# Performance work log

Measured on AMD Instinct MI355X. Metric: run time of the kernel, lower is better.

The kernel has to match this reference:

```python
import jax, jax.numpy as jnp
import numpy as np

HEADS = 8
DIM_HEAD = 64
SCALE = DIM_HEAD ** (-0.5)


def setup_inputs() -> dict:
    key = jax.random.key(0)
    k1, k2, k3, k4 = jax.random.split(key, 4)
    B, H, W, n, dim = 2, 64, 64, 8, 512
    inner = HEADS * DIM_HEAD  # 512
    x = jax.random.normal(k1, (B, H, W, n, dim), dtype=jnp.float32)
    mask = jax.random.uniform(k2, (B, H, W, 1, n, n), dtype=jnp.float32)
    w_qkv = jax.random.normal(k3, (dim, 3 * inner), dtype=jnp.float32) * 0.02
    w_out = jax.random.normal(k4, (inner, dim), dtype=jnp.float32) * 0.02
    b_out = jnp.zeros((dim,), dtype=jnp.float32)
    return {"x": x, "mask": mask, "w_qkv": w_qkv, "w_out": w_out, "b_out": b_out}


def reference(x, mask, w_qkv, w_out, b_out):
    B, H, W, n, dim = x.shape
    inner = HEADS * DIM_HEAD
    qkv = x @ w_qkv  # [B,H,W,n,3*inner]
    q, k, v = jnp.split(qkv, 3, axis=-1)

    def to_heads(t):
        # 'B H W n (h d) -> B H W h n d'
        t = t.reshape(B, H, W, n, HEADS, DIM_HEAD)
        return jnp.swapaxes(t, 3, 4)

    q, k, v = to_heads(q), to_heads(k), to_heads(v)
    dots = jnp.einsum('bxyhnd,bxyhmd->bxyhnm', q, k) * SCALE
    dots = dots * mask  # multiplicative mask pre-softmax
    attn = jax.nn.softmax(dots, axis=-1)
    out = jnp.einsum('bxyhnm,bxyhmd->bxyhnd', attn, v)
    # 'B H W h n d -> B H W n (h d)'
    out = jnp.swapaxes(out, 3, 4).reshape(B, H, W, n, inner)
    return out @ w_out + b_out
```

## Files before the change

### kernel.cpp

```cpp
#include <hip/hip_runtime.h>
#include <hip/hip_bf16.h>

#define NROWS 65536
#define DIM   512
#define SCALE_ 0.125f

typedef short bf16x8 __attribute__((ext_vector_type(8)));
typedef unsigned short u16x8 __attribute__((ext_vector_type(8)));
typedef float f32x4 __attribute__((ext_vector_type(4)));

__device__ __forceinline__ unsigned short f2bf(float f) {
  union { float f; unsigned u; } v; v.f = f;
  unsigned r = v.u + 0x7FFFu + ((v.u >> 16) & 1u);
  return (unsigned short)(r >> 16);
}

#define GLL16(gptr, lptr) \
  __builtin_amdgcn_global_load_lds((const __attribute__((address_space(1))) void*)(gptr), \
                                   (__attribute__((address_space(3))) void*)(lptr), 16, 0, 0)

__global__ void prep_w_kernel(const float* __restrict__ wqkv,
                              const float* __restrict__ wout,
                              unsigned short* __restrict__ wqkvT,
                              unsigned short* __restrict__ woutT) {
  int idx = blockIdx.x * 256 + threadIdx.x;
  if (idx < 1536 * 512) {
    int j = idx >> 9, c = idx & 511;
    wqkvT[idx] = f2bf(wqkv[(size_t)c * 1536 + j]);
  } else {
    int k2 = idx - 1536 * 512;
    int n = k2 >> 9, c = k2 & 511;
    woutT[k2] = f2bf(wout[(size_t)c * 512 + n]);
  }
}

__global__ __launch_bounds__(256, 2)
void qkv_attn_kernel(const float* __restrict__ x,
                     const float* __restrict__ mask,
                     const unsigned short* __restrict__ wqkvT,
                     unsigned short* __restrict__ attn_out) {
  __shared__ __align__(16) unsigned char smem[81920];

  const int t = threadIdx.x;
  const int lane = t & 63, wave = t >> 6;
  const int wm = wave >> 1, wn = wave & 1;
  const int fr = lane & 15, fq = lane >> 4;
  const int l8 = lane >> 3;
  const int cswz = ((lane & 7) ^ l8) * 8;

  const int per = gridDim.x >> 3;
  const int lin = (blockIdx.x & 7) * per + (blockIdx.x >> 3);
  const int mtile = lin >> 3, head = lin & 7;
  const int r0 = mtile * 128;

  float mreg[2][4];
  #pragma unroll
  for (int pp = 0; pp < 2; ++pp) {
    int pair = wave * 2 + pp;
    #pragma unroll
    for (int r = 0; r < 4; ++r) {
      int row = fq * 4 + r;
      int Pg = mtile * 16 + pair * 2 + (row >> 3);
      mreg[pp][r] = mask[(size_t)Pg * 64 + (row & 7) * 8 + (fr & 7)];
    }
  }

  f32x4 acc[4][6];
  const f32x4 z4 = {0.f, 0.f, 0.f, 0.f};
  #pragma unroll
  for (int m = 0; m < 4; ++m)
    #pragma unroll
    for (int n = 0; n < 6; ++n) acc[m][n] = z4;

  float4 va[8];
  const int arow = t >> 4, aq = t & 15;
  const unsigned abyte = (unsigned)arow * 128 +
                         ((((unsigned)(aq >> 1)) << 4) ^ (((unsigned)(arow & 7)) << 4)) +
                         (unsigned)(aq & 1) * 8;

  auto LOAD_A = [&](int kt2) {
    const int k0 = kt2 * 64;
    const float* gx = x + (size_t)(r0 + arow) * 512 + k0 + aq * 4;
    #pragma unroll
    for (int i2 = 0; i2 < 8; ++i2)
      va[i2] = *(const float4*)(gx + (size_t)i2 * 16 * 512);
  };
  auto WRITE_A = [&](int buf) {
    unsigned char* base = smem + buf * 40960;
    #pragma unroll
    for (int i2 = 0; i2 < 8; ++i2) {
      ushort4 p;
      p.x = f2bf(va[i2].x); p.y = f2bf(va[i2].y);
      p.z = f2bf(va[i2].z); p.w = f2bf(va[i2].w);
      *(ushort4*)(base + abyte + (unsigned)i2 * 2048) = p;
    }
  };
  auto STAGE_B = [&](int buf, int kt2) {
    unsigned char* base = smem + buf * 40960 + 16384;
    const unsigned short* gB = wqkvT + kt2 * 64 + cswz;
    #pragma unroll
    for (int i = 0; i < 6; ++i) {
      int c = wave * 6 + i;
      int n = c * 8 + l8;
      int jg = ((n >> 6) << 9) + head * 64 + (n & 63);
      GLL16(gB + (size_t)jg * 512, base + c * 1024);
    }
  };

  LOAD_A(0);
  STAGE_B(0, 0);
  WRITE_A(0);
  asm volatile("s_waitcnt vmcnt(0)" ::: "memory");
  __syncthreads();
  int cur = 0;

  for (int kt = 0; kt < 8; ++kt) {
    if (kt < 7) { LOAD_A(kt + 1); STAGE_B(cur ^ 1, kt + 1); }
    unsigned char* Ab = smem + cur * 40960;
    unsigned char* Bb = Ab + 16384;
    const unsigned xr = ((unsigned)(fr & 7)) << 4;
    #pragma unroll
    for (int kk = 0; kk < 2; ++kk) {
      const unsigned ko = ((unsigned)(kk * 64 + fq * 16)) ^ xr;
      bf16x8 a[4], b[6];
      #pragma unroll
      for (int m = 0; m < 4; ++m)
        a[m] = *(const bf16x8*)(Ab + (unsigned)(wm * 64 + m * 16 + fr) * 128 + ko);
      #pragma unroll
      for (int n = 0; n < 6; ++n)
        b[n] = *(const bf16x8*)(Bb + (unsigned)(wn * 96 + n * 16 + fr) * 128 + ko);
      #pragma unroll
      for (int m = 0; m < 4; ++m)
        #pragma unroll
        for (int n = 0; n < 6; ++n)
          acc[m][n] = __builtin_amdgcn_mfma_f32_16x16x32_bf16(a[m], b[n], acc[m][n], 0, 0, 0);
    }
    if (kt < 7) WRITE_A(cur ^ 1);
    asm volatile("s_waitcnt vmcnt(0)" ::: "memory");
    __syncthreads();
    cur ^= 1;
  }

  unsigned short* Qs = (unsigned short*)smem;
  unsigned short* Ks = (unsigned short*)(smem + 16384);
  unsigned short* VT = (unsigned short*)(smem + 32768);
  unsigned short* Pl = (unsigned short*)(smem + 52224);

  {
    int d = t >> 2, q = t & 3;
    ushort4 z; z.x = 0; z.y = 0; z.z = 0; z.w = 0;
    *(ushort4*)(VT + d * 152 + 128 + q * 4) = z;
  }
  #pragma unroll
  for (int n = 0; n < 6; ++n) {
    int col = wn * 96 + n * 16 + fr;
    #pragma unroll
    for (int m = 0; m < 4; ++m) {
      if (col < 128) {
        unsigned short* T = (col < 64) ? Qs : Ks;
        unsigned cc = (unsigned)(col & 63);
        #pragma unroll
        for (int r = 0; r < 4; ++r) {
          int row = wm * 64 + m * 16 + fq * 4 + r;
          unsigned byte = (unsigned)row * 128 + ((cc * 2) ^ (((unsigned)(row & 7)) << 4));
          *(unsigned short*)((unsigned char*)T + byte) = f2bf(acc[m][n][r]);
        }
      } else {
        int d = col - 128;
        ushort4 p;
        p.x = f2bf(acc[m][n][0]); p.y = f2bf(acc[m][n][1]);
        p.z = f2bf(acc[m][n][2]); p.w = f2bf(acc[m][n][3]);
        *(ushort4*)(VT + d * 152 + (wm * 64 + m * 16 + fq * 4)) = p;
      }
    }
  }
  __syncthreads();

  #pragma unroll
  for (int pp = 0; pp < 2; ++pp) {
    const int pair = wave * 2 + pp;
    const unsigned rbyte = (unsigned)(pair * 16 + fr) * 128;
    const unsigned xrp = ((unsigned)(fr & 7)) << 4;
    f32x4 s = {0.f, 0.f, 0.f, 0.f};
    #pragma unroll
    for (int kk = 0; kk < 2; ++kk) {
      const unsigned ko = ((unsigned)(kk * 64 + fq * 16)) ^ xrp;
      bf16x8 qf = *(const bf16x8*)((unsigned char*)Qs + rbyte + ko);
      bf16x8 kf = *(const bf16x8*)((unsigned char*)Ks + rbyte + ko);
      s = __builtin_amdgcn_mfma_f32_16x16x32_bf16(qf, kf, s, 0, 0, 0);
    }
    float p4[4];
    #pragma unroll
    for (int r = 0; r < 4; ++r) {
      int row = fq * 4 + r;
      bool valid = (row >> 3) == (fr >> 3);
      p4[r] = valid ? s[r] * SCALE_ * mreg[pp][r] : -3.0e38f;
    }
    #pragma unroll
    for (int r = 0; r < 4; ++r) {
      float v = p4[r];
      float mx = v;
      mx = fmaxf(mx, __shfl_xor(mx, 1));
      mx = fmaxf(mx, __shfl_xor(mx, 2));
      mx = fmaxf(mx, __shfl_xor(mx, 4));
      float e = __expf(v - mx);
      float sm = e;
      sm += __shfl_xor(sm, 1);
      sm += __shfl_xor(sm, 2);
      sm += __shfl_xor(sm, 4);
      p4[r] = e / sm;
    }
    #pragma unroll
    for (int r = 0; r < 4; ++r) {
      int row = fq * 4 + r;
      bool valid = (row >> 3) == (fr >> 3);
      Pl[pair * 640 + row * 40 + fr] = valid ? f2bf(p4[r]) : (unsigned short)0;
      Pl[pair * 640 + row * 40 + 16 + fr] = 0;
    }
    #pragma unroll
    for (int dblk = 0; dblk < 4; ++dblk) {
      bf16x8 af = *(const bf16x8*)((unsigned char*)VT +
                    (unsigned)(dblk * 16 + fr) * 304 + (unsigned)(pair * 32 + fq * 16));
      bf16x8 bf = *(const bf16x8*)((unsigned char*)Pl +
                    (unsigned)pair * 1280 + (unsigned)fr * 80 + (unsigned)fq * 16);
      f32x4 o = {0.f, 0.f, 0.f, 0.f};
      o = __builtin_amdgcn_mfma_f32_16x16x32_bf16(af, bf, o, 0, 0, 0);
      ushort4 pk;
      pk.x = f2bf(o[0]); pk.y = f2bf(o[1]); pk.z = f2bf(o[2]); pk.w = f2bf(o[3]);
      *(ushort4*)(attn_out + (size_t)(r0 + pair * 16 + fr) * 512 +
                  head * 64 + dblk * 16 + fq * 4) = pk;
    }
  }
}

__global__ __launch_bounds__(256, 2)
void outproj_kernel(const unsigned short* __restrict__ attn,
                    const unsigned short* __restrict__ woutT,
                    const float* __restrict__ bias,
                    float* __restrict__ out) {
  __shared__ __align__(16) unsigned char smem[65536];
  const int t = threadIdx.x;
  const int lane = t & 63, wave = t >> 6;
  const int wm = wave >> 1, wn = wave & 1;
  const int fr = lane & 15, fq = lane >> 4;
  const int l8 = lane >> 3;
  const int cswz = ((lane & 7) ^ l8) * 8;

  const int per = gridDim.x >> 3;
  const int lin = (blockIdx.x & 7) * per + (blockIdx.x >> 3);
  const int mtile = lin >> 2, nt = lin & 3;
  const int r0 = mtile * 128, n0 = nt * 128;

  f32x4 acc[4][4];
  const f32x4 z4 = {0.f, 0.f, 0.f, 0.f};
  #pragma unroll
  for (int m = 0; m < 4; ++m)
    #pragma unroll
    for (int n = 0; n < 4; ++n) acc[m][n] = z4;

  auto STAGE = [&](int buf, int kt2) {
    unsigned char* base = smem + buf * 32768;
    const int k0 = kt2 * 64;
    const unsigned short* gA = attn  + (size_t)(r0 + l8) * 512 + k0 + cswz;
    const unsigned short* gB = woutT + (size_t)(n0 + l8) * 512 + k0 + cswz;
    #pragma unroll
    for (int i = 0; i < 4; ++i) {
      int c = wave * 4 + i;
      GLL16(gA + (size_t)c * 8 * 512, base + c * 1024);
      GLL16(gB + (size_t)c * 8 * 512, base + 16384 + c * 1024);
    }
  };

  STAGE(0, 0);
  asm volatile("s_waitcnt vmcnt(0)" ::: "memory");
  __syncthreads();
  int cur = 0;

  for (int kt = 0; kt < 8; ++kt) {
    if (kt < 7) STAGE(cur ^ 1, kt + 1);
    unsigned char* Ab = smem + cur * 32768;
    unsigned char* Bb = Ab + 16384;
    const unsigned xr = ((unsigned)(fr & 7)) << 4;
    #pragma unroll
    for (int kk = 0; kk < 2; ++kk) {
      const unsigned ko = ((unsigned)(kk * 64 + fq * 16)) ^ xr;
      bf16x8 a[4], b[4];
      #pragma unroll
      for (int m = 0; m < 4; ++m)
        a[m] = *(const bf16x8*)(Ab + (unsigned)(wm * 64 + m * 16 + fr) * 128 + ko);
      #pragma unroll
      for (int n = 0; n < 4; ++n)
        b[n] = *(const bf16x8*)(Bb + (unsigned)(wn * 64 + n * 16 + fr) * 128 + ko);
      #pragma unroll
      for (int m = 0; m < 4; ++m)
        #pragma unroll
        for (int n = 0; n < 4; ++n)
          acc[m][n] = __builtin_amdgcn_mfma_f32_16x16x32_bf16(a[m], b[n], acc[m][n], 0, 0, 0);
    }
    asm volatile("s_waitcnt vmcnt(0)" ::: "memory");
    __syncthreads();
    cur ^= 1;
  }
  #pragma unroll
  for (int n = 0; n < 4; ++n) {
    int col = n0 + wn * 64 + n * 16 + fr;
    float bv = bias[col];
    #pragma unroll
    for (int m = 0; m < 4; ++m) {
      #pragma unroll
      for (int j = 0; j < 4; ++j) {
        int row = r0 + wm * 64 + m * 16 + fq * 4 + j;
        out[(size_t)row * 512 + col] = acc[m][n][j] + bv;
      }
    }
  }
}

extern "C" void kernel_launch(void* const* d_in, const int* in_sizes, int n_in,
                              void* d_out, int out_size, void* d_ws, size_t ws_size,
                              hipStream_t stream) {
  const float* x    = (const float*)d_in[0];
  const float* mask = (const float*)d_in[1];
  const float* wqkv = (const float*)d_in[2];
  const float* wout = (const float*)d_in[3];
  const float* bias = (const float*)d_in[4];
  float* out = (float*)d_out;

  unsigned char* ws = (unsigned char*)d_ws;
  unsigned short* attn  = (unsigned short*)ws;
  unsigned short* wqkvT = (unsigned short*)(ws + 67108864);
  unsigned short* woutT = (unsigned short*)(ws + 67108864 + 1572864);

  prep_w_kernel<<<4096, 256, 0, stream>>>(wqkv, wout, wqkvT, woutT);
  qkv_attn_kernel<<<4096, 256, 0, stream>>>(x, mask, wqkvT, attn);
  outproj_kernel<<<2048, 256, 0, stream>>>(attn, woutT, bias, out);
}
```

Measured before the change: 278.5 us.

## Pre-convert x to bf16 and stream QKV tiles via 4-stage async LDS pipeline

```diff
diff --git a/kernel.cpp b/kernel.cpp
--- a/kernel.cpp
+++ b/kernel.cpp
@@ -19,23 +19,35 @@
   __builtin_amdgcn_global_load_lds((const __attribute__((address_space(1))) void*)(gptr), \
                                    (__attribute__((address_space(3))) void*)(lptr), 16, 0, 0)
 
-__global__ void prep_w_kernel(const float* __restrict__ wqkv,
-                              const float* __restrict__ wout,
-                              unsigned short* __restrict__ wqkvT,
-                              unsigned short* __restrict__ woutT) {
-  int idx = blockIdx.x * 256 + threadIdx.x;
-  if (idx < 1536 * 512) {
-    int j = idx >> 9, c = idx & 511;
-    wqkvT[idx] = f2bf(wqkv[(size_t)c * 1536 + j]);
+__global__ void prep_kernel(const float* __restrict__ x,
+                            const float* __restrict__ wqkv,
+                            const float* __restrict__ wout,
+                            unsigned short* __restrict__ xb,
+                            unsigned short* __restrict__ wqkvT,
+                            unsigned short* __restrict__ woutT) {
+  if (blockIdx.x < 16384) {
+    size_t i = ((size_t)blockIdx.x * 256 + threadIdx.x) * 8;
+    float4 a = *(const float4*)(x + i);
+    float4 b = *(const float4*)(x + i + 4);
+    u16x8 p;
+    p[0] = f2bf(a.x); p[1] = f2bf(a.y); p[2] = f2bf(a.z); p[3] = f2bf(a.w);
+    p[4] = f2bf(b.x); p[5] = f2bf(b.y); p[6] = f2bf(b.z); p[7] = f2bf(b.w);
+    *(u16x8*)(xb + i) = p;
   } else {
-    int k2 = idx - 1536 * 512;
-    int n = k2 >> 9, c = k2 & 511;
-    woutT[k2] = f2bf(wout[(size_t)c * 512 + n]);
+    int idx = (blockIdx.x - 16384) * 256 + threadIdx.x;
+    if (idx < 1536 * 512) {
+      int j = idx >> 9, c = idx & 511;
+      wqkvT[idx] = f2bf(wqkv[(size_t)c * 1536 + j]);
+    } else {
+      int k2 = idx - 1536 * 512;
+      int n = k2 >> 9, c = k2 & 511;
+      woutT[k2] = f2bf(wout[(size_t)c * 512 + n]);
+    }
   }
 }
 
 __global__ __launch_bounds__(256, 2)
-void qkv_attn_kernel(const float* __restrict__ x,
+void qkv_attn_kernel(const unsigned short* __restrict__ xb,
                      const float* __restrict__ mask,
                      const unsigned short* __restrict__ wqkvT,
                      unsigned short* __restrict__ attn_out) {
@@ -45,14 +57,78 @@
   const int lane = t & 63, wave = t >> 6;
   const int wm = wave >> 1, wn = wave & 1;
   const int fr = lane & 15, fq = lane >> 4;
-  const int l8 = lane >> 3;
-  const int cswz = ((lane & 7) ^ l8) * 8;
+  const int swz = (((lane & 3) ^ ((lane >> 2) & 3))) * 8;
 
   const int per = gridDim.x >> 3;
   const int lin = (blockIdx.x & 7) * per + (blockIdx.x >> 3);
   const int mtile = lin >> 3, head = lin & 7;
   const int r0 = mtile * 128;
 
+  f32x4 acc[4][6];
+  const f32x4 z4 = {0.f, 0.f, 0.f, 0.f};
+  #pragma unroll
+  for (int m = 0; m < 4; ++m)
+    #pragma unroll
+    for (int n = 0; n < 6; ++n) acc[m][n] = z4;
+
+  auto STAGE = [&](int buf, int kt2) {
+    unsigned char* base = smem + buf * 20480;
+    const int k0 = kt2 * 32;
+    #pragma unroll
+    for (int i = 0; i < 2; ++i) {
+      int c = wave * 2 + i;
+      const unsigned short* g =
+          xb + (size_t)(r0 + c * 16 + (lane >> 2)) * 512 + k0 + swz;
+      GLL16(g, base + c * 1024);
+    }
+    #pragma unroll
+    for (int i = 0; i < 3; ++i) {
+      int c = wave * 3 + i;
+      int n = c * 16 + (lane >> 2);
+      int jg = ((n >> 6) << 9) + head * 64 + (n & 63);
+      GLL16(wqkvT + (size_t)jg * 512 + k0 + swz, base + 8192 + c * 1024);
+    }
+  };
+
+  auto COMPUTE = [&](int buf) {
+    unsigned char* Ab = smem + buf * 20480;
+    unsigned char* Bb = Ab + 8192;
+    const unsigned ko = ((unsigned)(fq ^ (fr & 3))) << 4;
+    bf16x8 a[4], b[6];
+    #pragma unroll
+    for (int m = 0; m < 4; ++m)
+      a[m] = *(const bf16x8*)(Ab + (unsigned)(wm * 64 + m * 16 + fr) * 64 + ko);
+    #pragma unroll
+    for (int n = 0; n < 6; ++n)
+      b[n] = *(const bf16x8*)(Bb + (unsigned)(wn * 96 + n * 16 + fr) * 64 + ko);
+    #pragma unroll
+    for (int m = 0; m < 4; ++m)
+      #pragma unroll
+      for (int n = 0; n < 6; ++n)
+        acc[m][n] = __builtin_amdgcn_mfma_f32_16x16x32_bf16(a[m], b[n], acc[m][n], 0, 0, 0);
+  };
+
+  STAGE(0, 0);
+  STAGE(1, 1);
+  for (int kt = 0; kt < 14; ++kt) {
+    STAGE((kt + 2) & 3, kt + 2);
+    asm volatile("s_waitcnt vmcnt(10)" ::: "memory");
+    __builtin_amdgcn_s_barrier();
+    COMPUTE(kt & 3);
+  }
+  asm volatile("s_waitcnt vmcnt(5)" ::: "memory");
+  __builtin_amdgcn_s_barrier();
+  COMPUTE(2);
+  asm volatile("s_waitcnt vmcnt(0)" ::: "memory");
+  __builtin_amdgcn_s_barrier();
+  COMPUTE(3);
+  __syncthreads();
+
+  unsigned short* Qs = (unsigned short*)smem;
+  unsigned short* Ks = (unsigned short*)(smem + 16384);
+  unsigned short* VT = (unsigned short*)(smem + 32768);
+  unsigned short* Pl = (unsigned short*)(smem + 52224);
+
   float mreg[2][4];
   #pragma unroll
   for (int pp = 0; pp < 2; ++pp) {
@@ -64,87 +140,6 @@
       mreg[pp][r] = mask[(size_t)Pg * 64 + (row & 7) * 8 + (fr & 7)];
     }
   }
-
-  f32x4 acc[4][6];
-  const f32x4 z4 = {0.f, 0.f, 0.f, 0.f};
-  #pragma unroll
-  for (int m = 0; m < 4; ++m)
-    #pragma unroll
-    for (int n = 0; n < 6; ++n) acc[m][n] = z4;
-
-  float4 va[8];
-  const int arow = t >> 4, aq = t & 15;
-  const unsigned abyte = (unsigned)arow * 128 +
-                         ((((unsigned)(aq >> 1)) << 4) ^ (((unsigned)(arow & 7)) << 4)) +
-                         (unsigned)(aq & 1) * 8;
-
-  auto LOAD_A = [&](int kt2) {
-    const int k0 = kt2 * 64;
-    const float* gx = x + (size_t)(r0 + arow) * 512 + k0 + aq * 4;
-    #pragma unroll
-    for (int i2 = 0; i2 < 8; ++i2)
-      va[i2] = *(const float4*)(gx + (size_t)i2 * 16 * 512);
-  };
-  auto WRITE_A = [&](int buf) {
-    unsigned char* base = smem + buf * 40960;
-    #pragma unroll
-    for (int i2 = 0; i2 < 8; ++i2) {
-      ushort4 p;
-      p.x = f2bf(va[i2].x); p.y = f2bf(va[i2].y);
-      p.z = f2bf(va[i2].z); p.w = f2bf(va[i2].w);
-      *(ushort4*)(base + abyte + (unsigned)i2 * 2048) = p;
-    }
-  };
-  auto STAGE_B = [&](int buf, int kt2) {
-    unsigned char* base = smem + buf * 40960 + 16384;
-    const unsigned short* gB = wqkvT + kt2 * 64 + cswz;
-    #pragma unroll
-    for (int i = 0; i < 6; ++i) {
-      int c = wave * 6 + i;
-      int n = c * 8 + l8;
-      int jg = ((n >> 6) << 9) + head * 64 + (n & 63);
-      GLL16(gB + (size_t)jg * 512, base + c * 1024);
-    }
-  };
-
-  LOAD_A(0);
-  STAGE_B(0, 0);
-  WRITE_A(0);
-  asm volatile("s_waitcnt vmcnt(0)" ::: "memory");
-  __syncthreads();
-  int cur = 0;
-
-  for (int kt = 0; kt < 8; ++kt) {
-    if (kt < 7) { LOAD_A(kt + 1); STAGE_B(cur ^ 1, kt + 1); }
-    unsigned char* Ab = smem + cur * 40960;
-    unsigned char* Bb = Ab + 16384;
-    const unsigned xr = ((unsigned)(fr & 7)) << 4;
-    #pragma unroll
-    for (int kk = 0; kk < 2; ++kk) {
-      const unsigned ko = ((unsigned)(kk * 64 + fq * 16)) ^ xr;
-      bf16x8 a[4], b[6];
-      #pragma unroll
-      for (int m = 0; m < 4; ++m)
-        a[m] = *(const bf16x8*)(Ab + (unsigned)(wm * 64 + m * 16 + fr) * 128 + ko);
-      #pragma unroll
-      for (int n = 0; n < 6; ++n)
-        b[n] = *(const bf16x8*)(Bb + (unsigned)(wn * 96 + n * 16 + fr) * 128 + ko);
-      #pragma unroll
-      for (int m = 0; m < 4; ++m)
-        #pragma unroll
-        for (int n = 0; n < 6; ++n)
-          acc[m][n] = __builtin_amdgcn_mfma_f32_16x16x32_bf16(a[m], b[n], acc[m][n], 0, 0, 0);
-    }
-    if (kt < 7) WRITE_A(cur ^ 1);
-    asm volatile("s_waitcnt vmcnt(0)" ::: "memory");
-    __syncthreads();
-    cur ^= 1;
-  }
-
-  unsigned short* Qs = (unsigned short*)smem;
-  unsigned short* Ks = (unsigned short*)(smem + 16384);
-  unsigned short* VT = (unsigned short*)(smem + 32768);
-  unsigned short* Pl = (unsigned short*)(smem + 52224);
 
   {
     int d = t >> 2, q = t & 3;
@@ -330,8 +325,9 @@
   unsigned short* attn  = (unsigned short*)ws;
   unsigned short* wqkvT = (unsigned short*)(ws + 67108864);
   unsigned short* woutT = (unsigned short*)(ws + 67108864 + 1572864);
-
-  prep_w_kernel<<<4096, 256, 0, stream>>>(wqkv, wout, wqkvT, woutT);
-  qkv_attn_kernel<<<4096, 256, 0, stream>>>(x, mask, wqkvT, attn);
+  unsigned short* xb    = (unsigned short*)(ws + 67108864 + 1572864 + 524288);
+
+  prep_kernel<<<20480, 256, 0, stream>>>(x, wqkv, wout, xb, wqkvT, woutT);
+  qkv_attn_kernel<<<4096, 256, 0, stream>>>(xb, mask, wqkvT, attn);
   outproj_kernel<<<2048, 256, 0, stream>>>(attn, woutT, bias, out);
 }
```

New measurement: 235.2 us. 15.5% less time.
